# Kernel tuning notes

Measured on AMD Instinct MI355X. Metric: run time of the kernel, lower is better.

The kernel has to match this reference:

```python
import jax, jax.numpy as jnp
import numpy as np

N = 8192      # nodes
E = 262144    # edges (avg degree 32)
F_IN = 128    # input node features
H = 4         # GAT heads
C = 64        # hidden_dim
HC = H * C    # 256, GAT concat width
ED = 3        # edge_dim
NC = 8        # num_classes
NEG_SLOPE = 0.2


def setup_inputs() -> dict:
    key = jax.random.key(0)
    ks = iter(jax.random.split(key, 40))
    def w(shape, scale=0.05):
        return jax.random.normal(next(ks), shape, jnp.float32) * scale
    return {
        "x": jax.random.normal(next(ks), (N, F_IN), jnp.float32),
        "edge_attr": jax.random.uniform(next(ks), (E, ED), dtype=jnp.float32),
        # GATConv params (PyG: lin/lin_edge have no bias, final bias is [H*C])
        "gat_lin_w": w((F_IN, HC)),
        "gat_lin_edge_w": w((ED, HC)),
        "att_src": w((H, C)), "att_dst": w((H, C)), "att_edge": w((H, C)),
        "gat_bias": jnp.zeros((HC,), jnp.float32),
        "norm1_g": jnp.ones((HC,), jnp.float32), "norm1_b": jnp.zeros((HC,), jnp.float32),
        # GraphRegularizer encoder: Linear(2*HC,HC) -> ELU -> Linear(HC,1)
        "reg_w1": w((2 * HC, HC)), "reg_b1": jnp.zeros((HC,), jnp.float32),
        "reg_w2": w((HC, 1)), "reg_b2": jnp.zeros((1,), jnp.float32),
        # ConfidenceGCNConv 1: lin(HC->C), conf_lin(ED->1)
        "g1_lin_w": w((HC, C)), "g1_lin_b": jnp.zeros((C,), jnp.float32),
        "g1_conf_w": w((ED, 1)), "g1_conf_b": jnp.zeros((1,), jnp.float32),
        "norm2_g": jnp.ones((C,), jnp.float32), "norm2_b": jnp.zeros((C,), jnp.float32),
        # ConfidenceGCNConv 2: lin(C->C)
        "g2_lin_w": w((C, C)), "g2_lin_b": jnp.zeros((C,), jnp.float32),
        "g2_conf_w": w((ED, 1)), "g2_conf_b": jnp.zeros((1,), jnp.float32),
        # classifier: Linear(C,C) -> ELU -> Dropout(eval) -> Linear(C,NC)
        "cls_w1": w((C, C)), "cls_b1": jnp.zeros((C,), jnp.float32),
        "cls_w2": w((C, NC)), "cls_b2": jnp.zeros((NC,), jnp.float32),
        "edge_index": jax.random.randint(next(ks), (2, E), 0, N),
        "batch": jnp.zeros((N,), jnp.int32),
    }


def _layernorm(x, g, b, eps=1e-5):
    mu = x.mean(-1, keepdims=True)
    var = ((x - mu) ** 2).mean(-1, keepdims=True)
    return (x - mu) * jax.lax.rsqrt(var + eps) * g + b


def _gat(x, edge_index, edge_attr, lin_w, lin_edge_w, att_src, att_dst, att_edge, bias):
    """PyG GATConv (concat heads, add_self_loops=True, edge self-loop attr = mean)."""
    loop = jnp.arange(N)
    row = jnp.concatenate([edge_index[0], loop])
    col = jnp.concatenate([edge_index[1], loop])
    ea = jnp.concatenate([edge_attr, jnp.broadcast_to(edge_attr.mean(0), (N, ED))], 0)
    xs = (x @ lin_w).reshape(N, H, C)                       # [N,H,C]
    a_src = (xs * att_src).sum(-1)                          # [N,H]
    a_dst = (xs * att_dst).sum(-1)
    xe = (ea @ lin_edge_w).reshape(-1, H, C)
    a_e = (xe * att_edge).sum(-1)                           # [E+N,H]
    alpha = jax.nn.leaky_relu(a_src[row] + a_dst[col] + a_e, NEG_SLOPE)
    amax = jax.ops.segment_max(alpha, col, num_segments=N)  # softmax over edges into dst
    alpha = jnp.exp(alpha - amax[col])
    denom = jax.ops.segment_sum(alpha, col, num_segments=N)
    alpha = alpha / (denom[col] + 1e-16)
    out = jax.ops.segment_sum(xs[row] * alpha[..., None], col, num_segments=N)
    return out.reshape(N, HC) + bias


def _conf_gcn(x, row, col, edge_attr, adj_recon, lin_w, lin_b, conf_w, conf_b):
    w = jax.nn.sigmoid(edge_attr @ conf_w + conf_b)[:, 0]   # [E]
    if adj_recon is not None:
        w = (w + adj_recon[row, col]) * 0.5
    deg = jax.ops.segment_sum(jnp.ones_like(w), row, num_segments=N)
    dinv = jnp.where(deg > 0, jax.lax.rsqrt(jnp.maximum(deg, 1e-12)), 0.0)
    norm = dinv[row] * dinv[col] * w
    out = jax.ops.segment_sum(x[row] * norm[:, None], col, num_segments=N)
    return out @ lin_w + lin_b


def _regularizer(node_emb, row, col, w1, b1, w2, b2):
    pair = jnp.concatenate([node_emb[row], node_emb[col]], axis=1)  # [E,2*HC]
    h = jax.nn.elu(pair @ w1 + b1)
    prob = jax.nn.sigmoid(h @ w2 + b2)[:, 0]
    diag = jnp.arange(N)
    adj = jnp.zeros((N, N), node_emb.dtype).at[row, col].set(prob)
    return adj.at[diag, diag].set(1.0)


def reference(x, edge_attr, gat_lin_w, gat_lin_edge_w, att_src, att_dst, att_edge,
              gat_bias, norm1_g, norm1_b, reg_w1, reg_b1, reg_w2, reg_b2,
              g1_lin_w, g1_lin_b, g1_conf_w, g1_conf_b, norm2_g, norm2_b,
              g2_lin_w, g2_lin_b, g2_conf_w, g2_conf_b,
              cls_w1, cls_b1, cls_w2, cls_b2, edge_index, batch):
    row, col = edge_index[0], edge_index[1]
    h = jax.nn.elu(_gat(x, edge_index, edge_attr, gat_lin_w, gat_lin_edge_w,
                        att_src, att_dst, att_edge, gat_bias))
    h = _layernorm(h, norm1_g, norm1_b)
    adj_recon = _regularizer(h, row, col, reg_w1, reg_b1, reg_w2, reg_b2)
    h = jax.nn.elu(_conf_gcn(h, row, col, edge_attr, adj_recon,
                             g1_lin_w, g1_lin_b, g1_conf_w, g1_conf_b))
    h = _layernorm(h, norm2_g, norm2_b)
    h = _conf_gcn(h, row, col, edge_attr, adj_recon,
                  g2_lin_w, g2_lin_b, g2_conf_w, g2_conf_b)
    logits = jax.nn.elu(h @ cls_w1 + cls_b1) @ cls_w2 + cls_b2  # dropout is eval-mode no-op
    # NOTE: the Python-level BFS path reconstruction (data-dependent, returns lists
    # of ints via .item() syncs) is intentionally omitted from the tensor reference.
    return (logits, adj_recon)
```

## Files before the change

### kernel.cpp

```cpp
#include <hip/hip_runtime.h>
#include <math.h>

#define NN 8192
#define NE 262144
#define FIN 128
#define HC 256
#define CC 64
#define NCLS 8
#define NDNT 16
#define ABNT 16

constexpr size_t OFF_XS    = 0;
constexpr size_t OFF_ASRC  = OFF_XS + (size_t)NN * 256;
constexpr size_t OFF_ADST  = OFF_ASRC + (size_t)NN * 4;
constexpr size_t OFF_ALPHA = OFF_ADST + (size_t)NN * 4;
constexpr size_t OFF_CONF1 = OFF_ALPHA + (size_t)NE * 4;
constexpr size_t OFF_CONF2 = OFF_CONF1 + (size_t)NE;
constexpr size_t OFF_COEF1 = OFF_CONF2 + (size_t)NE;
constexpr size_t OFF_COEF2 = OFF_COEF1 + (size_t)NE;
constexpr size_t OFF_H1    = OFF_COEF2 + (size_t)NE;
constexpr size_t OFF_A     = OFF_H1 + (size_t)NN * 256;
constexpr size_t OFF_B     = OFF_A + (size_t)NN * 256;
constexpr size_t OFF_H2    = OFF_B + (size_t)NN * 256;
constexpr size_t OFF_DINV  = OFF_H2 + (size_t)NN * 64;
constexpr size_t OFF_SUMEA = OFF_DINV + (size_t)NN;
constexpr size_t OFF_M     = OFF_SUMEA + 4;
constexpr size_t OFF_AELOOP= OFF_M + 12;
constexpr size_t OFF_INT   = OFF_AELOOP + 4;
constexpr size_t IOFF_DEGC   = 0;
constexpr size_t IOFF_DEGR   = IOFF_DEGC + NN;
constexpr size_t IOFF_COLOFF = IOFF_DEGR + NN;
constexpr size_t IOFF_CURSOR = IOFF_COLOFF + NN + 1;
constexpr size_t IOFF_CSRROW = IOFF_CURSOR + NN;
constexpr size_t IOFF_CSREID = IOFF_CSRROW + NE;

__device__ __forceinline__ float wave_sum(float v) {
    for (int o = 32; o; o >>= 1) v += __shfl_xor(v, o);
    return v;
}
__device__ __forceinline__ float wave_max(float v) {
    for (int o = 32; o; o >>= 1) v = fmaxf(v, __shfl_xor(v, o));
    return v;
}
__device__ __forceinline__ float eluf(float v) { return v > 0.f ? v : (expf(v) - 1.f); }
__device__ __forceinline__ float sigmf(float v) { return 1.f / (1.f + expf(-v)); }

__global__ __launch_bounds__(256) void k_init(int* deg_col, int* deg_row, float* sum_ea,
                                              float* adj, const float* lew,
                                              const float* att_edge, float* M) {
    int i = blockIdx.x * blockDim.x + threadIdx.x;
    deg_col[i] = 0;
    deg_row[i] = 0;
    adj[(size_t)i * NN + i] = 1.f;
    if (i < 3) sum_ea[i] = 0.f;
    if (i < 12) {
        int d = i >> 2, h = i & 3;
        float s = 0.f;
        for (int c = 0; c < 64; c++) s = fmaf(lew[d * 256 + h * 64 + c], att_edge[h * 64 + c], s);
        M[i] = s;
    }
}

__global__ __launch_bounds__(256) void k_node(const float* __restrict__ x, const float* __restrict__ W,
                                              const float* __restrict__ att_src, const float* __restrict__ att_dst,
                                              float* __restrict__ xs, float* __restrict__ a_src, float* __restrict__ a_dst) {
    __shared__ float xl[NDNT * FIN];
    int b = blockIdx.x, t = threadIdx.x;
    size_t base = (size_t)b * NDNT;
#pragma unroll
    for (int q = 0; q < NDNT * FIN / 256; ++q) {
        int idx = q * 256 + t;
        xl[idx] = x[base * FIN + idx];
    }
    __syncthreads();
    float acc[NDNT];
#pragma unroll
    for (int n = 0; n < NDNT; ++n) acc[n] = 0.f;
    for (int k = 0; k < FIN; ++k) {
        float wv = W[k * 256 + t];
#pragma unroll
        for (int n = 0; n < NDNT; ++n) acc[n] = fmaf(xl[n * FIN + k], wv, acc[n]);
    }
    float as = att_src[t], ad = att_dst[t];
#pragma unroll
    for (int n = 0; n < NDNT; ++n) {
        xs[(base + n) * 256 + t] = acc[n];
        float ps = wave_sum(acc[n] * as);
        float pd = wave_sum(acc[n] * ad);
        if ((t & 63) == 0) {
            a_src[(base + n) * 4 + (t >> 6)] = ps;
            a_dst[(base + n) * 4 + (t >> 6)] = pd;
        }
    }
}

__global__ __launch_bounds__(256) void k_edge(const int* __restrict__ ei, const float* __restrict__ eattr,
                                              const float* __restrict__ M,
                                              const float* __restrict__ a_src, const float* __restrict__ a_dst,
                                              const float* __restrict__ c1w, const float* __restrict__ c1b,
                                              const float* __restrict__ c2w, const float* __restrict__ c2b,
                                              float* __restrict__ alpha, float* __restrict__ conf1, float* __restrict__ conf2,
                                              int* __restrict__ deg_col, int* __restrict__ deg_row, float* __restrict__ sum_ea) {
    int e = blockIdx.x * 256 + threadIdx.x;
    int r = ei[e], c = ei[NE + e];
    float ea0 = eattr[e * 3 + 0], ea1 = eattr[e * 3 + 1], ea2 = eattr[e * 3 + 2];
#pragma unroll
    for (int h = 0; h < 4; h++) {
        float ae = fmaf(ea0, M[0 * 4 + h], fmaf(ea1, M[1 * 4 + h], ea2 * M[2 * 4 + h]));
        float v = a_src[r * 4 + h] + a_dst[c * 4 + h] + ae;
        alpha[(size_t)e * 4 + h] = v > 0.f ? v : 0.2f * v;
    }
    conf1[e] = sigmf(fmaf(ea0, c1w[0], fmaf(ea1, c1w[1], fmaf(ea2, c1w[2], c1b[0]))));
    conf2[e] = sigmf(fmaf(ea0, c2w[0], fmaf(ea1, c2w[1], fmaf(ea2, c2w[2], c2b[0]))));
    atomicAdd(&deg_col[c], 1);
    atomicAdd(&deg_row[r], 1);
    float s0 = wave_sum(ea0), s1 = wave_sum(ea1), s2 = wave_sum(ea2);
    if ((threadIdx.x & 63) == 0) {
        atomicAdd(&sum_ea[0], s0); atomicAdd(&sum_ea[1], s1); atomicAdd(&sum_ea[2], s2);
    }
}

__global__ __launch_bounds__(256) void k_loopdinv(const float* sum_ea, const float* M, float* aeloop,
                                                  const int* deg_row, float* dinv) {
    int i = blockIdx.x * blockDim.x + threadIdx.x;
    if (i < 4) {
        float m0 = sum_ea[0] * (1.f / NE), m1 = sum_ea[1] * (1.f / NE), m2 = sum_ea[2] * (1.f / NE);
        aeloop[i] = fmaf(m0, M[0 * 4 + i], fmaf(m1, M[1 * 4 + i], m2 * M[2 * 4 + i]));
    }
    int d = deg_row[i];
    dinv[i] = d > 0 ? rsqrtf((float)d) : 0.f;
}

__global__ __launch_bounds__(256) void k_scan(const int* __restrict__ deg_col, int* __restrict__ col_off, int* __restrict__ cursor) {
    __shared__ int sd[256];
    int t = threadIdx.x;
    int base_i = t * 32;
    int loc[32];
    int s = 0;
#pragma unroll
    for (int q = 0; q < 32; q++) { loc[q] = deg_col[base_i + q]; s += loc[q]; }
    sd[t] = s;
    __syncthreads();
    for (int d = 1; d < 256; d <<= 1) {
        int v = (t >= d) ? sd[t - d] : 0;
        __syncthreads();
        sd[t] += v;
        __syncthreads();
    }
    int acc = sd[t] - s;
#pragma unroll
    for (int q = 0; q < 32; q++) { col_off[base_i + q] = acc; cursor[base_i + q] = acc; acc += loc[q]; }
    if (t == 255) col_off[NN] = acc;
}

__global__ __launch_bounds__(256) void k_fill(const int* __restrict__ ei, int* __restrict__ cursor,
                                              int* __restrict__ csr_row, int* __restrict__ csr_eid) {
    int e = blockIdx.x * 256 + threadIdx.x;
    int r = ei[e], c = ei[NE + e];
    int pos = atomicAdd(&cursor[c], 1);
    csr_row[pos] = r;
    csr_eid[pos] = e;
}

__global__ __launch_bounds__(256) void k_gat(const int* __restrict__ col_off, const int* __restrict__ csr_row,
                                             const int* __restrict__ csr_eid,
                                             const float* __restrict__ alpha, const float* __restrict__ aeloop,
                                             const float* __restrict__ a_src, const float* __restrict__ a_dst,
                                             const float* __restrict__ xs, const float* __restrict__ gat_bias,
                                             const float* __restrict__ g, const float* __restrict__ b,
                                             float* __restrict__ h1) {
    int i = blockIdx.x, t = threadIdx.x, h = t >> 6, lane = t & 63;
    int beg = col_off[i], end = col_off[i + 1];
    __shared__ float m_s[4], s_s[4], red[8];
    __shared__ float wl[64][5];
    float sl = a_src[i * 4 + h] + a_dst[i * 4 + h] + aeloop[h];
    sl = sl > 0.f ? sl : 0.2f * sl;
    float mx = sl;
    for (int p = beg + lane; p < end; p += 64) mx = fmaxf(mx, alpha[(size_t)csr_eid[p] * 4 + h]);
    mx = wave_max(mx);
    float ss = (lane == 0) ? expf(sl - mx) : 0.f;
    for (int p = beg + lane; p < end; p += 64) ss += expf(alpha[(size_t)csr_eid[p] * 4 + h] - mx);
    ss = wave_sum(ss);
    if (lane == 0) { m_s[h] = mx; s_s[h] = ss; }
    __syncthreads();
    float minv = m_s[h];
    float sinv = 1.f / (s_s[h] + 1e-16f);
    float acc = expf(sl - minv) * sinv * xs[(size_t)i * 256 + t];
    for (int cb = beg; cb < end; cb += 64) {
        int ce = min(cb + 64, end);
        int p = cb + lane;
        if (p < ce) wl[lane][h] = expf(alpha[(size_t)csr_eid[p] * 4 + h] - minv) * sinv;
        __syncthreads();
        int n = ce - cb;
        for (int q = 0; q < n; ++q)
            acc = fmaf(wl[q][h], xs[(size_t)csr_row[cb + q] * 256 + t], acc);
        __syncthreads();
    }
    float v = eluf(acc + gat_bias[t]);
    float s1 = wave_sum(v), s2 = wave_sum(v * v);
    if (lane == 0) { red[h] = s1; red[4 + h] = s2; }
    __syncthreads();
    float mu = (red[0] + red[1] + red[2] + red[3]) * (1.f / 256.f);
    float m2 = (red[4] + red[5] + red[6] + red[7]) * (1.f / 256.f);
    float var = m2 - mu * mu;
    float rs = rsqrtf(var + 1e-5f);
    h1[(size_t)i * 256 + t] = (v - mu) * rs * g[t] + b[t];
}

__global__ __launch_bounds__(256) void k_AB(const float* __restrict__ h1, const float* __restrict__ w1,
                                            const float* __restrict__ b1, float* __restrict__ A, float* __restrict__ B) {
    __shared__ float hl[ABNT * 256];
    int bk = blockIdx.x, t = threadIdx.x;
    size_t base = (size_t)bk * ABNT;
#pragma unroll
    for (int n = 0; n < ABNT; ++n) hl[n * 256 + t] = h1[(base + n) * 256 + t];
    __syncthreads();
    float accA[ABNT], accB[ABNT];
    float bv = b1[t];
#pragma unroll
    for (int n = 0; n < ABNT; ++n) { accA[n] = bv; accB[n] = 0.f; }
    for (int k = 0; k < 256; ++k) {
        float wa = w1[k * 256 + t];
        float wb = w1[(256 + k) * 256 + t];
#pragma unroll
        for (int n = 0; n < ABNT; ++n) {
            float hv = hl[n * 256 + k];
            accA[n] = fmaf(hv, wa, accA[n]);
            accB[n] = fmaf(hv, wb, accB[n]);
        }
    }
#pragma unroll
    for (int n = 0; n < ABNT; ++n) {
        A[(base + n) * 256 + t] = accA[n];
        B[(base + n) * 256 + t] = accB[n];
    }
}

__global__ __launch_bounds__(256) void k_regc(const int* __restrict__ ei, const float* __restrict__ A,
                                              const float* __restrict__ B, const float* __restrict__ w2,
                                              const float* __restrict__ b2, const float* __restrict__ dinv,
                                              const float* __restrict__ conf1, const float* __restrict__ conf2,
                                              float* __restrict__ adj, float* __restrict__ coef1,
                                              float* __restrict__ coef2) {
    int t = threadIdx.x, lane = t & 63;
    int e = blockIdx.x * 4 + (t >> 6);
    int r = ei[e], c = ei[NE + e];
    const float4* A4 = (const float4*)(A + (size_t)r * 256);
    const float4* B4 = (const float4*)(B + (size_t)c * 256);
    float4 av = A4[lane], bv = B4[lane];
    float4 w4 = ((const float4*)w2)[lane];
    float v0 = eluf(av.x + bv.x), v1 = eluf(av.y + bv.y), v2 = eluf(av.z + bv.z), v3 = eluf(av.w + bv.w);
    float s = fmaf(v0, w4.x, fmaf(v1, w4.y, fmaf(v2, w4.z, v3 * w4.w)));
    s = wave_sum(s);
    if (lane == 0) {
        float p = sigmf(s + b2[0]);
        float adjv;
        if (r != c) { adj[(size_t)r * NN + c] = p; adjv = p; }
        else adjv = 1.f;
        float base = dinv[r] * dinv[c] * 0.5f;
        coef1[e] = base * (conf1[e] + adjv);
        coef2[e] = base * (conf2[e] + adjv);
    }
}

__global__ __launch_bounds__(256) void k_gcn1(const int* __restrict__ col_off, const int* __restrict__ csr_row,
                                              const int* __restrict__ csr_eid, const float* __restrict__ coef1,
                                              const float* __restrict__ h1, const float* __restrict__ W,
                                              const float* __restrict__ bias, const float* __restrict__ g,
                                              const float* __restrict__ bb, float* __restrict__ h2) {
    __shared__ float al[256];
    __shared__ float pl[256];
    int i = blockIdx.x, t = threadIdx.x;
    int beg = col_off[i], end = col_off[i + 1];
    float agg = 0.f;
    for (int p = beg; p < end; ++p)
        agg = fmaf(coef1[csr_eid[p]], h1[(size_t)csr_row[p] * 256 + t], agg);
    al[t] = agg;
    __syncthreads();
    int cc = t & 63, q = t >> 6;
    float part = 0.f;
#pragma unroll 4
    for (int k = q * 64; k < q * 64 + 64; k++) part = fmaf(al[k], W[k * 64 + cc], part);
    pl[t] = part;
    __syncthreads();
    if (t < 64) {
        float y = pl[t] + pl[t + 64] + pl[t + 128] + pl[t + 192] + bias[t];
        y = eluf(y);
        float s1 = wave_sum(y), s2 = wave_sum(y * y);
        float mu = s1 * (1.f / 64.f);
        float var = s2 * (1.f / 64.f) - mu * mu;
        h2[(size_t)i * 64 + t] = (y - mu) * rsqrtf(var + 1e-5f) * g[t] + bb[t];
    }
}

__global__ __launch_bounds__(256) void k_gcn2(const int* __restrict__ col_off, const int* __restrict__ csr_row,
                                              const int* __restrict__ csr_eid, const float* __restrict__ coef2,
                                              const float* __restrict__ h2, const float* __restrict__ g2w,
                                              const float* __restrict__ g2b, const float* __restrict__ cw1,
                                              const float* __restrict__ cb1, const float* __restrict__ cw2,
                                              const float* __restrict__ cb2, float* __restrict__ out) {
    __shared__ float zl[4][64];
    __shared__ float ul[4][64];
    __shared__ float tl[4][64];
    int t = threadIdx.x, w = t >> 6, lane = t & 63;
    int i = blockIdx.x * 4 + w;
    int beg = col_off[i], end = col_off[i + 1];
    float z = 0.f;
    for (int p = beg; p < end; ++p)
        z = fmaf(coef2[csr_eid[p]], h2[(size_t)csr_row[p] * 64 + lane], z);
    zl[w][lane] = z;
    __syncthreads();
    float u = g2b[lane];
#pragma unroll 4
    for (int k = 0; k < 64; k++) u = fmaf(zl[w][k], g2w[k * 64 + lane], u);
    ul[w][lane] = u;
    __syncthreads();
    float t1 = cb1[lane];
#pragma unroll 4
    for (int k = 0; k < 64; k++) t1 = fmaf(ul[w][k], cw1[k * 64 + lane], t1);
    t1 = eluf(t1);
    tl[w][lane] = t1;
    __syncthreads();
    if (lane < 8) {
        float o = cb2[lane];
#pragma unroll 4
        for (int k = 0; k < 64; k++) o = fmaf(tl[w][k], cw2[k * 8 + lane], o);
        out[(size_t)i * 8 + lane] = o;
    }
}

extern "C" void kernel_launch(void* const* d_in, const int* in_sizes, int n_in,
                              void* d_out, int out_size, void* d_ws, size_t ws_size,
                              hipStream_t stream) {
    const float* x           = (const float*)d_in[0];
    const float* edge_attr   = (const float*)d_in[1];
    const float* gat_lin_w   = (const float*)d_in[2];
    const float* gat_lin_edge_w = (const float*)d_in[3];
    const float* att_src     = (const float*)d_in[4];
    const float* att_dst     = (const float*)d_in[5];
    const float* att_edge    = (const float*)d_in[6];
    const float* gat_bias    = (const float*)d_in[7];
    const float* norm1_g     = (const float*)d_in[8];
    const float* norm1_b     = (const float*)d_in[9];
    const float* reg_w1      = (const float*)d_in[10];
    const float* reg_b1      = (const float*)d_in[11];
    const float* reg_w2      = (const float*)d_in[12];
    const float* reg_b2      = (const float*)d_in[13];
    const float* g1_lin_w    = (const float*)d_in[14];
    const float* g1_lin_b    = (const float*)d_in[15];
    const float* g1_conf_w   = (const float*)d_in[16];
    const float* g1_conf_b   = (const float*)d_in[17];
    const float* norm2_g     = (const float*)d_in[18];
    const float* norm2_b     = (const float*)d_in[19];
    const float* g2_lin_w    = (const float*)d_in[20];
    const float* g2_lin_b    = (const float*)d_in[21];
    const float* g2_conf_w   = (const float*)d_in[22];
    const float* g2_conf_b   = (const float*)d_in[23];
    const float* cls_w1      = (const float*)d_in[24];
    const float* cls_b1      = (const float*)d_in[25];
    const float* cls_w2      = (const float*)d_in[26];
    const float* cls_b2      = (const float*)d_in[27];
    const int*   edge_index  = (const int*)d_in[28];

    float* out = (float*)d_out;
    float* adj = out + (size_t)NN * NCLS;

    float* wsf   = (float*)d_ws;
    float* xs    = wsf + OFF_XS;
    float* a_src = wsf + OFF_ASRC;
    float* a_dst = wsf + OFF_ADST;
    float* alpha = wsf + OFF_ALPHA;
    float* conf1 = wsf + OFF_CONF1;
    float* conf2 = wsf + OFF_CONF2;
    float* coef1 = wsf + OFF_COEF1;
    float* coef2 = wsf + OFF_COEF2;
    float* h1    = wsf + OFF_H1;
    float* A     = wsf + OFF_A;
    float* B     = wsf + OFF_B;
    float* h2    = wsf + OFF_H2;
    float* dinv  = wsf + OFF_DINV;
    float* sum_ea= wsf + OFF_SUMEA;
    float* M     = wsf + OFF_M;
    float* aeloop= wsf + OFF_AELOOP;
    int* ib      = (int*)(wsf + OFF_INT);
    int* deg_col = ib + IOFF_DEGC;
    int* deg_row = ib + IOFF_DEGR;
    int* col_off = ib + IOFF_COLOFF;
    int* cursor  = ib + IOFF_CURSOR;
    int* csr_row = ib + IOFF_CSRROW;
    int* csr_eid = ib + IOFF_CSREID;

    hipMemsetAsync(adj, 0, (size_t)NN * NN * sizeof(float), stream);
    k_init<<<NN / 256, 256, 0, stream>>>(deg_col, deg_row, sum_ea, adj,
                                         gat_lin_edge_w, att_edge, M);
    k_node<<<NN / NDNT, 256, 0, stream>>>(x, gat_lin_w, att_src, att_dst, xs, a_src, a_dst);
    k_edge<<<NE / 256, 256, 0, stream>>>(edge_index, edge_attr, M, a_src, a_dst,
                                         g1_conf_w, g1_conf_b, g2_conf_w, g2_conf_b,
                                         alpha, conf1, conf2, deg_col, deg_row, sum_ea);
    k_loopdinv<<<NN / 256, 256, 0, stream>>>(sum_ea, M, aeloop, deg_row, dinv);
    k_scan<<<1, 256, 0, stream>>>(deg_col, col_off, cursor);
    k_fill<<<NE / 256, 256, 0, stream>>>(edge_index, cursor, csr_row, csr_eid);
    k_gat<<<NN, 256, 0, stream>>>(col_off, csr_row, csr_eid, alpha, aeloop, a_src, a_dst,
                                  xs, gat_bias, norm1_g, norm1_b, h1);
    k_AB<<<NN / ABNT, 256, 0, stream>>>(h1, reg_w1, reg_b1, A, B);
    k_regc<<<NE / 4, 256, 0, stream>>>(edge_index, A, B, reg_w2, reg_b2, dinv,
                                       conf1, conf2, adj, coef1, coef2);
    k_gcn1<<<NN, 256, 0, stream>>>(col_off, csr_row, csr_eid, coef1, h1,
                                   g1_lin_w, g1_lin_b, norm2_g, norm2_b, h2);
    k_gcn2<<<NN / 4, 256, 0, stream>>>(col_off, csr_row, csr_eid, coef2, h2,
                                       g2_lin_w, g2_lin_b, cls_w1, cls_b1, cls_w2, cls_b2, out);
    (void)in_sizes; (void)n_in; (void)out_size; (void)ws_size;
}
```

Measured before the change: 862.5 us.

## Add row-major CSR, restructure GAT/regc/gcn1 for vectorized gathers and row reuse

Result: slower. 904.2 us (+4.8%).

```diff
diff --git a/kernel.cpp b/kernel.cpp
--- a/kernel.cpp
+++ b/kernel.cpp
@@ -9,6 +9,7 @@
 #define NCLS 8
 #define NDNT 16
 #define ABNT 16
+#define G1NT 16
 
 constexpr size_t OFF_XS    = 0;
 constexpr size_t OFF_ASRC  = OFF_XS + (size_t)NN * 256;
@@ -27,12 +28,16 @@
 constexpr size_t OFF_M     = OFF_SUMEA + 4;
 constexpr size_t OFF_AELOOP= OFF_M + 12;
 constexpr size_t OFF_INT   = OFF_AELOOP + 4;
-constexpr size_t IOFF_DEGC   = 0;
-constexpr size_t IOFF_DEGR   = IOFF_DEGC + NN;
-constexpr size_t IOFF_COLOFF = IOFF_DEGR + NN;
-constexpr size_t IOFF_CURSOR = IOFF_COLOFF + NN + 1;
-constexpr size_t IOFF_CSRROW = IOFF_CURSOR + NN;
-constexpr size_t IOFF_CSREID = IOFF_CSRROW + NE;
+constexpr size_t IOFF_DEGC    = 0;
+constexpr size_t IOFF_DEGR    = IOFF_DEGC + NN;
+constexpr size_t IOFF_COLOFF  = IOFF_DEGR + NN;
+constexpr size_t IOFF_CURC    = IOFF_COLOFF + NN + 1;
+constexpr size_t IOFF_ROWOFF  = IOFF_CURC + NN;
+constexpr size_t IOFF_CURR    = IOFF_ROWOFF + NN + 1;
+constexpr size_t IOFF_CSR_ROW = IOFF_CURR + NN;
+constexpr size_t IOFF_CSR_EID = IOFF_CSR_ROW + NE;
+constexpr size_t IOFF_CSRR_COL= IOFF_CSR_EID + NE;
+constexpr size_t IOFF_CSRR_EID= IOFF_CSRR_COL + NE;
 
 __device__ __forceinline__ float wave_sum(float v) {
     for (int o = 32; o; o >>= 1) v += __shfl_xor(v, o);
@@ -131,14 +136,18 @@
     dinv[i] = d > 0 ? rsqrtf((float)d) : 0.f;
 }
 
-__global__ __launch_bounds__(256) void k_scan(const int* __restrict__ deg_col, int* __restrict__ col_off, int* __restrict__ cursor) {
+__global__ __launch_bounds__(256) void k_scan2(const int* __restrict__ deg_col, int* __restrict__ col_off, int* __restrict__ curC,
+                                               const int* __restrict__ deg_row, int* __restrict__ row_off, int* __restrict__ curR) {
+    const int* deg = (blockIdx.x == 0) ? deg_col : deg_row;
+    int* off = (blockIdx.x == 0) ? col_off : row_off;
+    int* cur = (blockIdx.x == 0) ? curC : curR;
     __shared__ int sd[256];
     int t = threadIdx.x;
     int base_i = t * 32;
     int loc[32];
     int s = 0;
 #pragma unroll
-    for (int q = 0; q < 32; q++) { loc[q] = deg_col[base_i + q]; s += loc[q]; }
+    for (int q = 0; q < 32; q++) { loc[q] = deg[base_i + q]; s += loc[q]; }
     sd[t] = s;
     __syncthreads();
     for (int d = 1; d < 256; d <<= 1) {
@@ -149,17 +158,22 @@
     }
     int acc = sd[t] - s;
 #pragma unroll
-    for (int q = 0; q < 32; q++) { col_off[base_i + q] = acc; cursor[base_i + q] = acc; acc += loc[q]; }
-    if (t == 255) col_off[NN] = acc;
-}
-
-__global__ __launch_bounds__(256) void k_fill(const int* __restrict__ ei, int* __restrict__ cursor,
-                                              int* __restrict__ csr_row, int* __restrict__ csr_eid) {
+    for (int q = 0; q < 32; q++) { off[base_i + q] = acc; cur[base_i + q] = acc; acc += loc[q]; }
+    if (t == 255) off[NN] = acc;
+}
+
+__global__ __launch_bounds__(256) void k_fill(const int* __restrict__ ei, int* __restrict__ curC,
+                                              int* __restrict__ csr_row, int* __restrict__ csr_eid,
+                                              int* __restrict__ curR, int* __restrict__ csrR_col,
+                                              int* __restrict__ csrR_eid) {
     int e = blockIdx.x * 256 + threadIdx.x;
     int r = ei[e], c = ei[NE + e];
-    int pos = atomicAdd(&cursor[c], 1);
+    int pos = atomicAdd(&curC[c], 1);
     csr_row[pos] = r;
     csr_eid[pos] = e;
+    int posR = atomicAdd(&curR[r], 1);
+    csrR_col[posR] = c;
+    csrR_eid[posR] = e;
 }
 
 __global__ __launch_bounds__(256) void k_gat(const int* __restrict__ col_off, const int* __restrict__ csr_row,
@@ -169,10 +183,11 @@
                                              const float* __restrict__ xs, const float* __restrict__ gat_bias,
                                              const float* __restrict__ g, const float* __restrict__ b,
                                              float* __restrict__ h1) {
-    int i = blockIdx.x, t = threadIdx.x, h = t >> 6, lane = t & 63;
+    int i = blockIdx.x, t = threadIdx.x, h = t >> 6, lane = t & 63, w = t >> 6;
     int beg = col_off[i], end = col_off[i + 1];
     __shared__ float m_s[4], s_s[4], red[8];
     __shared__ float wl[64][5];
+    __shared__ float accL[4 * 260];
     float sl = a_src[i * 4 + h] + a_dst[i * 4 + h] + aeloop[h];
     sl = sl > 0.f ? sl : 0.2f * sl;
     float mx = sl;
@@ -185,20 +200,33 @@
     __syncthreads();
     float minv = m_s[h];
     float sinv = 1.f / (s_s[h] + 1e-16f);
-    float acc = expf(sl - minv) * sinv * xs[(size_t)i * 256 + t];
+    float4 acc = make_float4(0.f, 0.f, 0.f, 0.f);
+    int hh = lane >> 4;
     for (int cb = beg; cb < end; cb += 64) {
         int ce = min(cb + 64, end);
+        int n = ce - cb;
         int p = cb + lane;
         if (p < ce) wl[lane][h] = expf(alpha[(size_t)csr_eid[p] * 4 + h] - minv) * sinv;
         __syncthreads();
-        int n = ce - cb;
-        for (int q = 0; q < n; ++q)
-            acc = fmaf(wl[q][h], xs[(size_t)csr_row[cb + q] * 256 + t], acc);
+        for (int q = w; q < n; q += 4) {
+            int r = csr_row[cb + q];
+            float wt = wl[q][hh];
+            float4 xv = ((const float4*)(xs + (size_t)r * 256))[lane];
+            acc.x = fmaf(wt, xv.x, acc.x);
+            acc.y = fmaf(wt, xv.y, acc.y);
+            acc.z = fmaf(wt, xv.z, acc.z);
+            acc.w = fmaf(wt, xv.w, acc.w);
+        }
         __syncthreads();
     }
-    float v = eluf(acc + gat_bias[t]);
+    ((float4*)(accL + w * 260))[lane] = acc;
+    __syncthreads();
+    float v = accL[t] + accL[260 + t] + accL[520 + t] + accL[780 + t];
+    float wself = expf(sl - minv) * sinv;
+    v = fmaf(wself, xs[(size_t)i * 256 + t], v);
+    v = eluf(v + gat_bias[t]);
     float s1 = wave_sum(v), s2 = wave_sum(v * v);
-    if (lane == 0) { red[h] = s1; red[4 + h] = s2; }
+    if (lane == 0) { red[w] = s1; red[4 + w] = s2; }
     __syncthreads();
     float mu = (red[0] + red[1] + red[2] + red[3]) * (1.f / 256.f);
     float m2 = (red[4] + red[5] + red[6] + red[7]) * (1.f / 256.f);
@@ -236,30 +264,37 @@
     }
 }
 
-__global__ __launch_bounds__(256) void k_regc(const int* __restrict__ ei, const float* __restrict__ A,
-                                              const float* __restrict__ B, const float* __restrict__ w2,
-                                              const float* __restrict__ b2, const float* __restrict__ dinv,
+__global__ __launch_bounds__(256) void k_regc(const int* __restrict__ row_off, const int* __restrict__ csrR_col,
+                                              const int* __restrict__ csrR_eid,
+                                              const float* __restrict__ A, const float* __restrict__ B,
+                                              const float* __restrict__ w2, const float* __restrict__ b2,
+                                              const float* __restrict__ dinv,
                                               const float* __restrict__ conf1, const float* __restrict__ conf2,
                                               float* __restrict__ adj, float* __restrict__ coef1,
                                               float* __restrict__ coef2) {
-    int t = threadIdx.x, lane = t & 63;
-    int e = blockIdx.x * 4 + (t >> 6);
-    int r = ei[e], c = ei[NE + e];
-    const float4* A4 = (const float4*)(A + (size_t)r * 256);
-    const float4* B4 = (const float4*)(B + (size_t)c * 256);
-    float4 av = A4[lane], bv = B4[lane];
+    int t = threadIdx.x, w = t >> 6, lane = t & 63;
+    int r = blockIdx.x * 4 + w;
+    float4 av = ((const float4*)(A + (size_t)r * 256))[lane];
     float4 w4 = ((const float4*)w2)[lane];
-    float v0 = eluf(av.x + bv.x), v1 = eluf(av.y + bv.y), v2 = eluf(av.z + bv.z), v3 = eluf(av.w + bv.w);
-    float s = fmaf(v0, w4.x, fmaf(v1, w4.y, fmaf(v2, w4.z, v3 * w4.w)));
-    s = wave_sum(s);
-    if (lane == 0) {
-        float p = sigmf(s + b2[0]);
-        float adjv;
-        if (r != c) { adj[(size_t)r * NN + c] = p; adjv = p; }
-        else adjv = 1.f;
-        float base = dinv[r] * dinv[c] * 0.5f;
-        coef1[e] = base * (conf1[e] + adjv);
-        coef2[e] = base * (conf2[e] + adjv);
+    float b2v = b2[0];
+    float dr = dinv[r];
+    int beg = row_off[r], end = row_off[r + 1];
+    for (int p = beg; p < end; ++p) {
+        int c = csrR_col[p];
+        int e = csrR_eid[p];
+        float4 bv = ((const float4*)(B + (size_t)c * 256))[lane];
+        float v0 = eluf(av.x + bv.x), v1 = eluf(av.y + bv.y);
+        float v2 = eluf(av.z + bv.z), v3 = eluf(av.w + bv.w);
+        float s = fmaf(v0, w4.x, fmaf(v1, w4.y, fmaf(v2, w4.z, v3 * w4.w)));
+        s = wave_sum(s);
+        if (lane == 0) {
+            float pv = sigmf(s + b2v);
+            float adjv = 1.f;
+            if (r != c) { adj[(size_t)r * NN + c] = pv; adjv = pv; }
+            float base = dr * dinv[c] * 0.5f;
+            coef1[e] = base * (conf1[e] + adjv);
+            coef2[e] = base * (conf2[e] + adjv);
+        }
     }
 }
 
@@ -268,29 +303,52 @@
                                               const float* __restrict__ h1, const float* __restrict__ W,
                                               const float* __restrict__ bias, const float* __restrict__ g,
                                               const float* __restrict__ bb, float* __restrict__ h2) {
-    __shared__ float al[256];
-    __shared__ float pl[256];
-    int i = blockIdx.x, t = threadIdx.x;
-    int beg = col_off[i], end = col_off[i + 1];
-    float agg = 0.f;
-    for (int p = beg; p < end; ++p)
-        agg = fmaf(coef1[csr_eid[p]], h1[(size_t)csr_row[p] * 256 + t], agg);
-    al[t] = agg;
-    __syncthreads();
-    int cc = t & 63, q = t >> 6;
-    float part = 0.f;
-#pragma unroll 4
-    for (int k = q * 64; k < q * 64 + 64; k++) part = fmaf(al[k], W[k * 64 + cc], part);
-    pl[t] = part;
-    __syncthreads();
-    if (t < 64) {
-        float y = pl[t] + pl[t + 64] + pl[t + 128] + pl[t + 192] + bias[t];
-        y = eluf(y);
-        float s1 = wave_sum(y), s2 = wave_sum(y * y);
-        float mu = s1 * (1.f / 64.f);
-        float var = s2 * (1.f / 64.f) - mu * mu;
-        h2[(size_t)i * 64 + t] = (y - mu) * rsqrtf(var + 1e-5f) * g[t] + bb[t];
-    }
+    __shared__ float agg[G1NT * 260];
+    int t = threadIdx.x, w = t >> 6, lane = t & 63;
+    size_t ibase = (size_t)blockIdx.x * G1NT;
+#pragma unroll
+    for (int s = 0; s < 4; ++s) {
+        int n = w * 4 + s;
+        int i = ibase + n;
+        int beg = col_off[i], end = col_off[i + 1];
+        float4 acc = make_float4(0.f, 0.f, 0.f, 0.f);
+        for (int p = beg; p < end; ++p) {
+            float cf = coef1[csr_eid[p]];
+            float4 hv = ((const float4*)(h1 + (size_t)csr_row[p] * 256))[lane];
+            acc.x = fmaf(cf, hv.x, acc.x);
+            acc.y = fmaf(cf, hv.y, acc.y);
+            acc.z = fmaf(cf, hv.z, acc.z);
+            acc.w = fmaf(cf, hv.w, acc.w);
+        }
+        ((float4*)(agg + n * 260))[lane] = acc;
+    }
+    __syncthreads();
+    int n2 = t >> 4, q = t & 15;
+    const float* aggn = agg + n2 * 260;
+    float4 y = ((const float4*)bias)[q];
+    for (int k = 0; k < 256; ++k) {
+        float a = aggn[k];
+        float4 wv = ((const float4*)(W + k * 64))[q];
+        y.x = fmaf(a, wv.x, y.x);
+        y.y = fmaf(a, wv.y, y.y);
+        y.z = fmaf(a, wv.z, y.z);
+        y.w = fmaf(a, wv.w, y.w);
+    }
+    y.x = eluf(y.x); y.y = eluf(y.y); y.z = eluf(y.z); y.w = eluf(y.w);
+    float s1 = y.x + y.y + y.z + y.w;
+    float s2 = y.x * y.x + y.y * y.y + y.z * y.z + y.w * y.w;
+#pragma unroll
+    for (int o = 1; o < 16; o <<= 1) { s1 += __shfl_xor(s1, o); s2 += __shfl_xor(s2, o); }
+    float mu = s1 * (1.f / 64.f);
+    float var = s2 * (1.f / 64.f) - mu * mu;
+    float rs = rsqrtf(var + 1e-5f);
+    float4 g4 = ((const float4*)g)[q], b4 = ((const float4*)bb)[q];
+    float4 outv;
+    outv.x = (y.x - mu) * rs * g4.x + b4.x;
+    outv.y = (y.y - mu) * rs * g4.y + b4.y;
+    outv.z = (y.z - mu) * rs * g4.z + b4.z;
+    outv.w = (y.w - mu) * rs * g4.w + b4.w;
+    ((float4*)(h2 + (ibase + n2) * 64))[q] = outv;
 }
 
 __global__ __launch_bounds__(256) void k_gcn2(const int* __restrict__ col_off, const int* __restrict__ csr_row,
@@ -386,9 +444,13 @@
     int* deg_col = ib + IOFF_DEGC;
     int* deg_row = ib + IOFF_DEGR;
     int* col_off = ib + IOFF_COLOFF;
-    int* cursor  = ib + IOFF_CURSOR;
-    int* csr_row = ib + IOFF_CSRROW;
-    int* csr_eid = ib + IOFF_CSREID;
+    int* curC    = ib + IOFF_CURC;
+    int* row_off = ib + IOFF_ROWOFF;
+    int* curR    = ib + IOFF_CURR;
+    int* csr_row = ib + IOFF_CSR_ROW;
+    int* csr_eid = ib + IOFF_CSR_EID;
+    int* csrR_col= ib + IOFF_CSRR_COL;
+    int* csrR_eid= ib + IOFF_CSRR_EID;
 
     hipMemsetAsync(adj, 0, (size_t)NN * NN * sizeof(float), stream);
     k_init<<<NN / 256, 256, 0, stream>>>(deg_col, deg_row, sum_ea, adj,
@@ -398,15 +460,15 @@
                                          g1_conf_w, g1_conf_b, g2_conf_w, g2_conf_b,
                                          alpha, conf1, conf2, deg_col, deg_row, sum_ea);
     k_loopdinv<<<NN / 256, 256, 0, stream>>>(sum_ea, M, aeloop, deg_row, dinv);
-    k_scan<<<1, 256, 0, stream>>>(deg_col, col_off, cursor);
-    k_fill<<<NE / 256, 256, 0, stream>>>(edge_index, cursor, csr_row, csr_eid);
+    k_scan2<<<2, 256, 0, stream>>>(deg_col, col_off, curC, deg_row, row_off, curR);
+    k_fill<<<NE / 256, 256, 0, stream>>>(edge_index, curC, csr_row, csr_eid, curR, csrR_col, csrR_eid);
     k_gat<<<NN, 256, 0, stream>>>(col_off, csr_row, csr_eid, alpha, aeloop, a_src, a_dst,
                                   xs, gat_bias, norm1_g, norm1_b, h1);
     k_AB<<<NN / ABNT, 256, 0, stream>>>(h1, reg_w1, reg_b1, A, B);
-    k_regc<<<NE / 4, 256, 0, stream>>>(edge_index, A, B, reg_w2, reg_b2, dinv,
-                                       conf1, conf2, adj, coef1, coef2);
-    k_gcn1<<<NN, 256, 0, stream>>>(col_off, csr_row, csr_eid, coef1, h1,
-                                   g1_lin_w, g1_lin_b, norm2_g, norm2_b, h2);
+    k_regc<<<NN / 4, 256, 0, stream>>>(row_off, csrR_col, csrR_eid, A, B, reg_w2, reg_b2,
+                                       dinv, conf1, conf2, adj, coef1, coef2);
+    k_gcn1<<<NN / G1NT, 256, 0, stream>>>(col_off, csr_row, csr_eid, coef1, h1,
+                                          g1_lin_w, g1_lin_b, norm2_g, norm2_b, h2);
     k_gcn2<<<NN / 4, 256, 0, stream>>>(col_off, csr_row, csr_eid, coef2, h2,
                                        g2_lin_w, g2_lin_b, cls_w1, cls_b1, cls_w2, cls_b2, out);
     (void)in_sizes; (void)n_in; (void)out_size; (void)ws_size;
```
